# Optimization experiments

Hardware: AMD Instinct MI355X
Metric: run time of the kernel (lower is better)

The kernel has to match this reference:

```python
import jax, jax.numpy as jnp
import numpy as np

N, E, G = 50000, 1600000, 64          # nodes, edges, graphs
NODE_IN, EDGE_IN, HID, L, H = 32, 16, 64, 3, 4
C = HID // H                           # per-head channels (PyG out_channels)


def setup_inputs() -> dict:
    key = jax.random.key(0)
    ks = jax.random.split(key, 12)
    x = jax.random.normal(ks[0], (N, NODE_IN), jnp.float32)
    edge_index = jax.random.randint(ks[1], (2, E), 0, N, jnp.int32)
    edge_attr = jax.random.normal(ks[2], (E, EDGE_IN), jnp.float32)
    batch = jnp.sort(jax.random.randint(ks[3], (N,), 0, G, jnp.int32))
    s = lambda k, shape, fan: jax.random.normal(k, shape, jnp.float32) / np.sqrt(fan)
    Wn = s(ks[4], (NODE_IN, HID), NODE_IN); bn = jnp.zeros((HID,), jnp.float32)
    Wq = s(ks[5], (L, HID, HID), HID);      bq = jnp.zeros((L, HID), jnp.float32)
    Wk = s(ks[6], (L, HID, HID), HID);      bk = jnp.zeros((L, HID), jnp.float32)
    Wv = s(ks[7], (L, HID, HID), HID);      bv = jnp.zeros((L, HID), jnp.float32)
    We = s(ks[8], (L, EDGE_IN, HID), EDGE_IN)          # lin_edge, bias=False in PyG
    Ws = s(ks[9], (L, HID, HID), HID);      bs = jnp.zeros((L, HID), jnp.float32)  # lin_skip
    W1 = s(ks[10], (HID, HID // 2), HID);   b1 = jnp.zeros((HID // 2,), jnp.float32)
    W2 = s(ks[11], (HID // 2, 1), HID // 2); b2 = jnp.zeros((1,), jnp.float32)
    return dict(x=x, edge_index=edge_index, edge_attr=edge_attr, batch=batch,
                Wn=Wn, bn=bn, Wq=Wq, bq=bq, Wk=Wk, bk=bk, Wv=Wv, bv=bv,
                We=We, Ws=Ws, bs=bs, W1=W1, b1=b1, W2=W2, b2=b2)


def _transformer_conv(x, src, dst, edge_attr, Wq, bq, Wk, bk, Wv, bv, We, Ws, bs):
    # PyG TransformerConv (concat=True, beta=False, root_weight=True), eval mode.
    q = (x @ Wq + bq)[dst].reshape(E, H, C)              # query at target nodes
    e = (edge_attr @ We).reshape(E, H, C)                # edge embedding
    k = (x @ Wk + bk)[src].reshape(E, H, C) + e          # key at source + edge
    alpha = (q * k).sum(-1) / jnp.sqrt(jnp.float32(C))   # [E, H]
    amax = jax.ops.segment_max(alpha, dst, num_segments=N)
    ex = jnp.exp(alpha - amax[dst])
    denom = jax.ops.segment_sum(ex, dst, num_segments=N)
    attn = ex / (denom[dst] + 1e-16)                     # segment softmax over in-edges
    v = (x @ Wv + bv)[src].reshape(E, H, C) + e
    agg = jax.ops.segment_sum((v * attn[..., None]).reshape(E, HID), dst, num_segments=N)
    return agg + x @ Ws + bs                             # skip connection (lin_skip)


def reference(x, edge_index, edge_attr, batch, Wn, bn, Wq, bq, Wk, bk, Wv, bv,
              We, Ws, bs, W1, b1, W2, b2):
    src, dst = edge_index[0], edge_index[1]
    h = jax.nn.relu(x @ Wn + bn)
    for l in range(L):  # dropout is identity in eval mode
        h_new = jax.nn.relu(_transformer_conv(h, src, dst, edge_attr,
                                              Wq[l], bq[l], Wk[l], bk[l],
                                              Wv[l], bv[l], We[l], Ws[l], bs[l]))
        h = h + h_new
    # global_mean_pool
    cnt = jax.ops.segment_sum(jnp.ones((N,), h.dtype), batch, num_segments=G)
    pooled = jax.ops.segment_sum(h, batch, num_segments=G) / jnp.maximum(cnt, 1.0)[:, None]
    out = jax.nn.relu(pooled @ W1 + b1) @ W2 + b2
    return out.squeeze(-1)
```

## Files before the change

### kernel.cpp

```cpp
#include <hip/hip_runtime.h>
#include <hip/hip_fp16.h>
#include <stdint.h>

#define Nn 50000
#define Ee 1600000
#define Gg 64
#define TB 2048
#define NTB ((Ee + TB - 1) / TB)
#define NBK ((Nn + 255) / 256)

typedef _Float16 f16x2 __attribute__((ext_vector_type(2)));
typedef _Float16 f16x4 __attribute__((ext_vector_type(4)));

__device__ __forceinline__ float fdot2f(f16x2 a, f16x2 b, float c) {
#if __has_builtin(__builtin_amdgcn_fdot2)
    return __builtin_amdgcn_fdot2(a, b, c, false);
#else
    return fmaf((float)a[0], (float)b[0], fmaf((float)a[1], (float)b[1], c));
#endif
}

__global__ void k_hist(const int* __restrict__ ei, int* __restrict__ deg) {
    int e = blockIdx.x * blockDim.x + threadIdx.x;
    if (e < Ee) atomicAdd(&deg[ei[Ee + e]], 1);
}

__global__ void k_scan1(const int* __restrict__ deg, int* __restrict__ row_ptr,
                        int* __restrict__ bsum) {
    __shared__ int buf[256];
    int i = blockIdx.x * 256 + threadIdx.x;
    int v = (i < Nn) ? deg[i] : 0;
    buf[threadIdx.x] = v;
    __syncthreads();
    for (int off = 1; off < 256; off <<= 1) {
        int t = (threadIdx.x >= off) ? buf[threadIdx.x - off] : 0;
        __syncthreads();
        buf[threadIdx.x] += t;
        __syncthreads();
    }
    if (i < Nn) row_ptr[i + 1] = buf[threadIdx.x];
    if (threadIdx.x == 255) bsum[blockIdx.x] = buf[255];
}

__global__ void k_scan2(int* __restrict__ bsum, int nb) {
    __shared__ int buf[256];
    int v = (threadIdx.x < nb) ? bsum[threadIdx.x] : 0;
    buf[threadIdx.x] = v;
    __syncthreads();
    for (int off = 1; off < 256; off <<= 1) {
        int t = (threadIdx.x >= off) ? buf[threadIdx.x - off] : 0;
        __syncthreads();
        buf[threadIdx.x] += t;
        __syncthreads();
    }
    if (threadIdx.x < nb) bsum[threadIdx.x] = buf[threadIdx.x];
}

__global__ void k_scan3(int* __restrict__ row_ptr, const int* __restrict__ bsum) {
    int i = blockIdx.x * 256 + threadIdx.x;
    if (i > Nn) return;
    if (i == 0) { row_ptr[0] = 0; return; }
    int b = (i - 1) >> 8;
    if (b > 0) row_ptr[i] += bsum[b - 1];
}

__global__ void k_scatter(const int* __restrict__ ei, int* __restrict__ cursor,
                          int* __restrict__ src_perm, int* __restrict__ eperm) {
    int e = blockIdx.x * blockDim.x + threadIdx.x;
    if (e >= Ee) return;
    int dst = ei[Ee + e];
    int pos = atomicAdd(&cursor[dst], 1);
    src_perm[pos] = ei[e];
    eperm[pos] = e;
}

__global__ void k_easort(const float* __restrict__ ea, const int* __restrict__ eperm,
                         __half* __restrict__ ea_h) {
    long t = (long)blockIdx.x * blockDim.x + threadIdx.x;
    if (t >= (long)Ee * 4) return;
    long idx = t >> 2;
    int e = eperm[idx];
    float4 v = ((const float4*)ea)[(long)e * 4 + (t & 3)];
    __half2 lo = __floats2half2_rn(v.x, v.y);
    __half2 hi = __floats2half2_rn(v.z, v.w);
    ((__half2*)ea_h)[t * 2]     = lo;
    ((__half2*)ea_h)[t * 2 + 1] = hi;
}


__global__ __launch_bounds__(256) void k_cnt(const int* __restrict__ ei,
                                             int* __restrict__ table) {
    __shared__ int hist[NBK];
    for (int i = threadIdx.x; i < NBK; i += 256) hist[i] = 0;
    __syncthreads();
    int e0 = blockIdx.x * TB;
    for (int i = threadIdx.x; i < TB; i += 256) {
        int e = e0 + i;
        if (e >= Ee) break;
        atomicAdd(&hist[ei[Ee + e] >> 8], 1);
    }
    __syncthreads();
    for (int i = threadIdx.x; i < NBK; i += 256)
        table[i * NTB + blockIdx.x] = hist[i];
}

__global__ __launch_bounds__(256) void k_colscan(int* __restrict__ table,
                                                 int* __restrict__ bktsz) {
    __shared__ int buf[1024];
    int c = blockIdx.x;
    for (int k = 0; k < 4; ++k) {
        int i = threadIdx.x + k * 256;
        buf[i] = (i < NTB) ? table[c * NTB + i] : 0;
    }
    __syncthreads();
    for (int off = 1; off < 1024; off <<= 1) {
        int v[4];
        for (int k = 0; k < 4; ++k) {
            int i = threadIdx.x + k * 256;
            v[k] = (i >= off) ? buf[i - off] : 0;
        }
        __syncthreads();
        for (int k = 0; k < 4; ++k) buf[threadIdx.x + k * 256] += v[k];
        __syncthreads();
    }
    for (int k = 0; k < 4; ++k) {
        int i = threadIdx.x + k * 256;
        if (i < NTB) table[c * NTB + i] = i ? buf[i - 1] : 0;
    }
    if (threadIdx.x == 0) bktsz[c] = buf[1023];
}

__global__ __launch_bounds__(256) void k_bktscan(const int* __restrict__ bktsz,
                                                 int* __restrict__ bktbase) {
    __shared__ int buf[256];
    int i = threadIdx.x;
    buf[i] = (i < NBK) ? bktsz[i] : 0;
    __syncthreads();
    for (int off = 1; off < 256; off <<= 1) {
        int v = (i >= off) ? buf[i - off] : 0;
        __syncthreads();
        buf[i] += v;
        __syncthreads();
    }
    if (i == 0) bktbase[0] = 0;
    if (i < NBK) bktbase[i + 1] = buf[i];
}

__global__ __launch_bounds__(256) void k_binfill(const int* __restrict__ ei,
                        const int* __restrict__ table, const int* __restrict__ bktbase,
                        unsigned long long* __restrict__ tmp) {
    __shared__ int off_s[NBK];
    __shared__ int cnt_s[NBK];
    for (int i = threadIdx.x; i < NBK; i += 256) {
        off_s[i] = table[i * NTB + blockIdx.x];
        cnt_s[i] = 0;
    }
    __syncthreads();
    int e0 = blockIdx.x * TB;
    for (int i = threadIdx.x; i < TB; i += 256) {
        int e = e0 + i;
        if (e >= Ee) break;
        int src = ei[e];
        int dst = ei[Ee + e];
        int b = dst >> 8;
        int r = atomicAdd(&cnt_s[b], 1);
        long pos = (long)bktbase[b] + off_s[b] + r;
        tmp[pos] = ((unsigned long long)(unsigned)dst << 37)
                 | ((unsigned long long)(unsigned)src << 21)
                 | (unsigned long long)(unsigned)e;
    }
}

__global__ __launch_bounds__(256) void k_bktB(const unsigned long long* __restrict__ tmp,
                        const int* __restrict__ bktbase, int* __restrict__ row_ptr,
                        unsigned long long* __restrict__ tmp2) {
    __shared__ int cnt[256];
    __shared__ int sc[256];
    __shared__ int lro[256];
    int b = blockIdx.x, tid = threadIdx.x;
    cnt[tid] = 0;
    __syncthreads();
    int s = bktbase[b], t_end = bktbase[b + 1];
    for (int i = s + tid; i < t_end; i += 256)
        atomicAdd(&cnt[(int)(tmp[i] >> 37) & 255], 1);
    __syncthreads();
    sc[tid] = cnt[tid];
    __syncthreads();
    for (int off = 1; off < 256; off <<= 1) {
        int v = (tid >= off) ? sc[tid - off] : 0;
        __syncthreads();
        sc[tid] += v;
        __syncthreads();
    }
    lro[tid] = tid ? sc[tid - 1] : 0;
    cnt[tid] = 0;
    int n = b * 256 + tid;
    if (n < Nn) row_ptr[n] = s + lro[tid];
    if (b == NBK - 1 && tid == 0) row_ptr[Nn] = Ee;
    __syncthreads();
    for (int i = s + tid; i < t_end; i += 256) {
        unsigned long long p = tmp[i];
        int dn = (int)(p >> 37) & 255;
        int r = atomicAdd(&cnt[dn], 1);
        int pos = s + lro[dn] + r;
        tmp2[pos] = (((p >> 21) & 0xFFFFull) << 32) | (p & 0x1FFFFFull);
    }
}

__global__ void k_scatB(const unsigned long long* __restrict__ tmp2,
                        int* __restrict__ src_perm,
                        const float* __restrict__ ea, __half* __restrict__ ea_h) {
    int t = blockIdx.x * blockDim.x + threadIdx.x;
    if (t >= Ee) return;
    unsigned long long p = tmp2[t];
    src_perm[t] = (int)(p >> 32);
    int e = (int)(p & 0xFFFFFFFFull);
    const float4* er = (const float4*)(ea + (size_t)e * 16);
    float4 v0 = er[0], v1 = er[1], v2 = er[2], v3 = er[3];
    __half2 h0 = __floats2half2_rn(v0.x, v0.y), h1 = __floats2half2_rn(v0.z, v0.w);
    __half2 h2 = __floats2half2_rn(v1.x, v1.y), h3 = __floats2half2_rn(v1.z, v1.w);
    __half2 h4 = __floats2half2_rn(v2.x, v2.y), h5 = __floats2half2_rn(v2.z, v2.w);
    __half2 h6 = __floats2half2_rn(v3.x, v3.y), h7 = __floats2half2_rn(v3.z, v3.w);
    uint4 a = make_uint4(*(unsigned*)&h0, *(unsigned*)&h1,
                         *(unsigned*)&h2, *(unsigned*)&h3);
    uint4 bb = make_uint4(*(unsigned*)&h4, *(unsigned*)&h5,
                          *(unsigned*)&h6, *(unsigned*)&h7);
    uint4* o = (uint4*)(ea_h + (size_t)t * 16);
    o[0] = a;
    o[1] = bb;
}

__global__ void k_gbound(const int* __restrict__ batch, int* __restrict__ gstart) {
    int n = blockIdx.x * blockDim.x + threadIdx.x;
    if (n >= Nn) return;
    int b = batch[n];
    if (n == 0) { for (int g = 0; g <= b; ++g) gstart[g] = 0; }
    else { int bp = batch[n - 1]; for (int g = bp + 1; g <= b; ++g) gstart[g] = n; }
    if (n == Nn - 1) { for (int g = b + 1; g <= Gg; ++g) gstart[g] = Nn; }
}

__global__ __launch_bounds__(256) void k_encode(const float* __restrict__ x,
                         const float* __restrict__ Wn,
                         const float* __restrict__ bn, float* __restrict__ h) {
    __shared__ float sx[64 * 32];
    int base = blockIdx.x * 64;
    for (int i = threadIdx.x; i < 512; i += 256) {
        int off = i * 4, row = off >> 5;
        float4 v = (base + row < Nn) ? ((const float4*)(x))[(base * 32 + off) >> 2]
                                     : make_float4(0.f, 0.f, 0.f, 0.f);
        ((float4*)sx)[i] = v;
    }
    __syncthreads();
    int lane = threadIdx.x & 63, wv = threadIdx.x >> 6;
    float acc[16];
    float b = bn[lane];
#pragma unroll
    for (int nn = 0; nn < 16; ++nn) acc[nn] = b;
#pragma unroll 1
    for (int k0 = 0; k0 < 32; k0 += 4) {
        float w0 = Wn[(k0 + 0) * 64 + lane];
        float w1 = Wn[(k0 + 1) * 64 + lane];
        float w2 = Wn[(k0 + 2) * 64 + lane];
        float w3 = Wn[(k0 + 3) * 64 + lane];
#pragma unroll
        for (int nn = 0; nn < 16; ++nn) {
            int row = wv * 16 + nn;
            float4 hv = *(const float4*)&sx[row * 32 + k0];
            acc[nn] = fmaf(hv.x, w0, fmaf(hv.y, w1, fmaf(hv.z, w2, fmaf(hv.w, w3, acc[nn]))));
        }
    }
#pragma unroll
    for (int nn = 0; nn < 16; ++nn) {
        int n = base + wv * 16 + nn;
        if (n < Nn) h[(size_t)n * 64 + lane] = fmaxf(acc[nn], 0.f);
    }
}

__global__ void k_wqm3(const float* __restrict__ Wq_all, const float* __restrict__ bq_all,
                       const float* __restrict__ We_all, float* __restrict__ Wqm3,
                       float* __restrict__ bqm3) {
    int l = blockIdx.x;
    const float* Wq = Wq_all + l * 4096;
    const float* bq = bq_all + l * 64;
    const float* We = We_all + l * 1024;
    float* Wqm = Wqm3 + l * 4096;
    float* bqm = bqm3 + l * 64;
    for (int o = threadIdx.x; o < 64 * 64; o += 256) {
        int j = o >> 6, lp = o & 63, hh = lp >> 4, ii = lp & 15;
        float acc = 0.f;
#pragma unroll
        for (int c = 0; c < 16; ++c)
            acc += Wq[j * 64 + hh * 16 + c] * We[ii * 64 + hh * 16 + c];
        Wqm[o] = acc;
    }
    if (threadIdx.x < 64) {
        int hh = threadIdx.x >> 4, ii = threadIdx.x & 15;
        float acc = 0.f;
#pragma unroll
        for (int c = 0; c < 16; ++c)
            acc += bq[hh * 16 + c] * We[ii * 64 + hh * 16 + c];
        bqm[threadIdx.x] = acc;
    }
}

__global__ __launch_bounds__(256) void k_qkvt(const float* __restrict__ h,
                       const float* __restrict__ Wq, const float* __restrict__ bq,
                       const float* __restrict__ Wk, const float* __restrict__ bk,
                       const float* __restrict__ Wv, const float* __restrict__ bv,
                       const float* __restrict__ Wqm, const float* __restrict__ bqm,
                       const float* __restrict__ Ws, const float* __restrict__ bs,
                       float* __restrict__ qn, __half* __restrict__ kv,
                       float* __restrict__ tq, float* __restrict__ sn) {
    __shared__ float sh[64 * 64];
    int base = blockIdx.x * 64;
    for (int i = threadIdx.x; i < 1024; i += 256) {
        int off = i * 4, row = off >> 6;
        float4 v = (base + row < Nn) ? ((const float4*)(h))[((size_t)base * 64 + off) >> 2]
                                     : make_float4(0.f, 0.f, 0.f, 0.f);
        ((float4*)sh)[i] = v;
    }
    __syncthreads();
    int lane = threadIdx.x & 63, wv = threadIdx.x >> 6;
    float aq[16], ak[16], av[16], at[16], as_[16];
    float _bq = bq[lane], _bk = bk[lane], _bv = bv[lane], _bt = bqm[lane], _bs = bs[lane];
#pragma unroll
    for (int nn = 0; nn < 16; ++nn) {
        aq[nn] = _bq; ak[nn] = _bk; av[nn] = _bv; at[nn] = _bt; as_[nn] = _bs;
    }
#pragma unroll 1
    for (int k0 = 0; k0 < 64; k0 += 4) {
        float wq[4], wk[4], wvv[4], wt[4], ws[4];
#pragma unroll
        for (int j = 0; j < 4; ++j) {
            wq[j] = Wq[(k0 + j) * 64 + lane];
            wk[j] = Wk[(k0 + j) * 64 + lane];
            wvv[j] = Wv[(k0 + j) * 64 + lane];
            wt[j] = Wqm[(k0 + j) * 64 + lane];
            ws[j] = Ws[(k0 + j) * 64 + lane];
        }
#pragma unroll
        for (int nn = 0; nn < 16; ++nn) {
            int row = wv * 16 + nn;
            float4 hv = *(const float4*)&sh[row * 64 + k0];
            aq[nn] = fmaf(hv.x, wq[0], fmaf(hv.y, wq[1], fmaf(hv.z, wq[2], fmaf(hv.w, wq[3], aq[nn]))));
            ak[nn] = fmaf(hv.x, wk[0], fmaf(hv.y, wk[1], fmaf(hv.z, wk[2], fmaf(hv.w, wk[3], ak[nn]))));
            av[nn] = fmaf(hv.x, wvv[0], fmaf(hv.y, wvv[1], fmaf(hv.z, wvv[2], fmaf(hv.w, wvv[3], av[nn]))));
            at[nn] = fmaf(hv.x, wt[0], fmaf(hv.y, wt[1], fmaf(hv.z, wt[2], fmaf(hv.w, wt[3], at[nn]))));
            as_[nn] = fmaf(hv.x, ws[0], fmaf(hv.y, ws[1], fmaf(hv.z, ws[2], fmaf(hv.w, ws[3], as_[nn]))));
        }
    }
#pragma unroll
    for (int nn = 0; nn < 16; ++nn) {
        int n = base + wv * 16 + nn;
        if (n < Nn) {
            size_t o = (size_t)n * 64 + lane;
            qn[o] = aq[nn]; tq[o] = at[nn]; sn[o] = as_[nn];
            kv[(size_t)n * 128 + lane]      = __float2half_rn(ak[nn]);
            kv[(size_t)n * 128 + 64 + lane] = __float2half_rn(av[nn]);
        }
    }
}

__global__ __launch_bounds__(256) void k_layer4(float* __restrict__ h,
                      const float* __restrict__ qn, const __half* __restrict__ kv,
                      const float* __restrict__ tq, const float* __restrict__ sn,
                      const int* __restrict__ row_ptr, const int* __restrict__ src_perm,
                      const __half* __restrict__ eah, const float* __restrict__ We) {
    __shared__ float sWe[1024];
    __shared__ float tE[4][64];
    __shared__ float tV[4][64];
    for (int t = threadIdx.x; t < 1024; t += 256) sWe[t] = We[t];
    __syncthreads();
    int lane = threadIdx.x & 63, wv = threadIdx.x >> 6;
    int slot = lane >> 4, sl = lane & 15;
    int n = blockIdx.x * 4 + wv;
    if (n >= Nn) return;
    int beg = row_ptr[n], end = row_ptr[n + 1];
    const float SC = 0.25f * 1.4426950408889634f;
    float4 q4 = *(const float4*)&qn[(size_t)n * 64 + 4 * sl];
    float4 t4 = *(const float4*)&tq[(size_t)n * 64 + 4 * sl];
    f16x2 qa = {(_Float16)(q4.x * SC), (_Float16)(q4.y * SC)};
    f16x2 qb = {(_Float16)(q4.z * SC), (_Float16)(q4.w * SC)};
    f16x2 ta = {(_Float16)(t4.x * SC), (_Float16)(t4.y * SC)};
    f16x2 tb = {(_Float16)(t4.z * SC), (_Float16)(t4.w * SC)};
    const int xoff = 4 * (sl & 3);
    float accd = 0.f;
    float4 accv = make_float4(0.f, 0.f, 0.f, 0.f);
    float4 acce = make_float4(0.f, 0.f, 0.f, 0.f);
    for (int idx = beg; idx < end; idx += 8) {
        int e0 = idx + slot, e1 = idx + 4 + slot;
        bool ok0 = e0 < end, ok1 = e1 < end;
        int i0 = ok0 ? e0 : beg, i1 = ok1 ? e1 : beg;
        int s0 = src_perm[i0], s1 = src_perm[i1];
        f16x4 k0 = *(const f16x4*)(kv + (size_t)s0 * 128 + 4 * sl);
        f16x4 v0 = *(const f16x4*)(kv + (size_t)s0 * 128 + 64 + 4 * sl);
        f16x4 k1 = *(const f16x4*)(kv + (size_t)s1 * 128 + 4 * sl);
        f16x4 v1 = *(const f16x4*)(kv + (size_t)s1 * 128 + 64 + 4 * sl);
        f16x4 x0 = *(const f16x4*)(eah + (size_t)i0 * 16 + xoff);
        f16x4 x1 = *(const f16x4*)(eah + (size_t)i1 * 16 + xoff);
        float a0 = fdot2f(qa, __builtin_shufflevector(k0, k0, 0, 1),
                   fdot2f(qb, __builtin_shufflevector(k0, k0, 2, 3),
                   fdot2f(ta, __builtin_shufflevector(x0, x0, 0, 1),
                   fdot2f(tb, __builtin_shufflevector(x0, x0, 2, 3), -6.0f))));
        float a1 = fdot2f(qa, __builtin_shufflevector(k1, k1, 0, 1),
                   fdot2f(qb, __builtin_shufflevector(k1, k1, 2, 3),
                   fdot2f(ta, __builtin_shufflevector(x1, x1, 0, 1),
                   fdot2f(tb, __builtin_shufflevector(x1, x1, 2, 3), -6.0f))));
        a0 += __shfl_xor(a0, 1, 4); a1 += __shfl_xor(a1, 1, 4);
        a0 += __shfl_xor(a0, 2, 4); a1 += __shfl_xor(a1, 2, 4);
        float p0 = ok0 ? __builtin_exp2f(a0) : 0.f;
        float p1 = ok1 ? __builtin_exp2f(a1) : 0.f;
        accd += p0 + p1;
        accv.x = fmaf(p0, (float)v0[0], fmaf(p1, (float)v1[0], accv.x));
        accv.y = fmaf(p0, (float)v0[1], fmaf(p1, (float)v1[1], accv.y));
        accv.z = fmaf(p0, (float)v0[2], fmaf(p1, (float)v1[2], accv.z));
        accv.w = fmaf(p0, (float)v0[3], fmaf(p1, (float)v1[3], accv.w));
        acce.x = fmaf(p0, (float)x0[0], fmaf(p1, (float)x1[0], acce.x));
        acce.y = fmaf(p0, (float)x0[1], fmaf(p1, (float)x1[1], acce.y));
        acce.z = fmaf(p0, (float)x0[2], fmaf(p1, (float)x1[2], acce.z));
        acce.w = fmaf(p0, (float)x0[3], fmaf(p1, (float)x1[3], acce.w));
    }
    accd   += __shfl_xor(accd, 16);   accd   += __shfl_xor(accd, 32);
    accv.x += __shfl_xor(accv.x, 16); accv.x += __shfl_xor(accv.x, 32);
    accv.y += __shfl_xor(accv.y, 16); accv.y += __shfl_xor(accv.y, 32);
    accv.z += __shfl_xor(accv.z, 16); accv.z += __shfl_xor(accv.z, 32);
    accv.w += __shfl_xor(accv.w, 16); accv.w += __shfl_xor(accv.w, 32);
    acce.x += __shfl_xor(acce.x, 16); acce.x += __shfl_xor(acce.x, 32);
    acce.y += __shfl_xor(acce.y, 16); acce.y += __shfl_xor(acce.y, 32);
    acce.z += __shfl_xor(acce.z, 16); acce.z += __shfl_xor(acce.z, 32);
    acce.w += __shfl_xor(acce.w, 16); acce.w += __shfl_xor(acce.w, 32);
    float inv = 1.f / (accd + 1e-16f);
    if (slot == 0) {
        ((float4*)tE[wv])[sl] = make_float4(acce.x * inv, acce.y * inv,
                                            acce.z * inv, acce.w * inv);
        ((float4*)tV[wv])[sl] = make_float4(accv.x * inv, accv.y * inv,
                                            accv.z * inv, accv.w * inv);
    }
    int hh = lane >> 4;
    float re = 0.f;
#pragma unroll
    for (int i = 0; i < 16; ++i)
        re = fmaf(tE[wv][hh * 16 + i], sWe[i * 64 + lane], re);
    size_t o = (size_t)n * 64 + lane;
    float hv = h[o];
    h[o] = hv + fmaxf(tV[wv][lane] + re + sn[o], 0.f);
}

template <bool SORTED>
__global__ __launch_bounds__(256) void k_layer(float* __restrict__ h,
                      const float* __restrict__ qn, const __half* __restrict__ kv,
                      const float* __restrict__ tq, const float* __restrict__ sn,
                      const int* __restrict__ row_ptr, const int* __restrict__ src_perm,
                      const int* __restrict__ eperm, const __half* __restrict__ eah,
                      const float* __restrict__ eaf, const float* __restrict__ We) {
    __shared__ float sWe[1024];
    __shared__ float tile[4][64];
    for (int t = threadIdx.x; t < 1024; t += 256) sWe[t] = We[t];
    __syncthreads();
    int lane = threadIdx.x & 63, wv = threadIdx.x >> 6;
    int hh = lane >> 4, cc = lane & 15;
    int n = blockIdx.x * 4 + wv;
    if (n >= Nn) return;
    int beg = row_ptr[n], end = row_ptr[n + 1];
    const float SC = 0.25f * 1.4426950408889634f;
    float q = qn[(size_t)n * 64 + lane] * SC;
    float t = tq[(size_t)n * 64 + lane] * SC;
    float m = -INFINITY, accd = 0.f, accv = 0.f, acce = 0.f;
    int idx = beg;
    for (; idx < end; ++idx) {
        long b0 = (long)src_perm[idx] * 128;
        float k0 = __half2float(kv[b0 + lane]);
        float v0 = __half2float(kv[b0 + 64 + lane]);
        float x0 = SORTED ? __half2float(eah[(long)idx * 16 + cc])
                          : eaf[(long)eperm[idx] * 16 + cc];
        float a0 = fmaf(q, k0, x0 * t);
        a0 += __shfl_xor(a0, 1, 16);
        a0 += __shfl_xor(a0, 2, 16);
        a0 += __shfl_xor(a0, 4, 16);
        a0 += __shfl_xor(a0, 8, 16);
        float nm = fmaxf(m, a0);
        float w = __builtin_exp2f(m - nm);
        float p0 = __builtin_exp2f(a0 - nm);
        accd = fmaf(accd, w, p0);
        accv = fmaf(accv, w, p0 * v0);
        acce = fmaf(acce, w, p0 * x0);
        m = nm;
    }
    float inv = 1.f / (accd + 1e-16f);
    tile[wv][lane] = acce * inv;
    float re = 0.f;
#pragma unroll
    for (int i = 0; i < 16; ++i)
        re = fmaf(tile[wv][hh * 16 + i], sWe[i * 64 + lane], re);
    size_t o = (size_t)n * 64 + lane;
    float hv = h[o];
    h[o] = hv + fmaxf(fmaf(accv, inv, re + sn[o]), 0.f);
}

__global__ void k_pool(const float* __restrict__ h, const int* __restrict__ gstart,
                       const float* __restrict__ W1, const float* __restrict__ b1,
                       const float* __restrict__ W2, const float* __restrict__ b2,
                       float* __restrict__ out) {
    int g = blockIdx.x;
    int lane = threadIdx.x & 63, wv = threadIdx.x >> 6;
    int beg = gstart[g], end = gstart[g + 1];
    __shared__ float red[4][64];
    __shared__ float sp[64];
    __shared__ float sh[32];
    float acc = 0.f;
    for (int n = beg + wv; n < end; n += 4) acc += h[(size_t)n * 64 + lane];
    red[wv][lane] = acc;
    __syncthreads();
    if (threadIdx.x < 64) {
        float c = fmaxf((float)(end - beg), 1.f);
        sp[lane] = (red[0][lane] + red[1][lane] + red[2][lane] + red[3][lane]) / c;
    }
    __syncthreads();
    if (threadIdx.x < 32) {
        int t = threadIdx.x;
        float a = b1[t];
#pragma unroll
        for (int i = 0; i < 64; ++i) a = fmaf(sp[i], W1[i * 32 + t], a);
        sh[t] = fmaxf(a, 0.f) * W2[t];
    }
    __syncthreads();
    if (threadIdx.x == 0) {
        float s = b2[0];
#pragma unroll
        for (int i = 0; i < 32; ++i) s += sh[i];
        out[g] = s;
    }
}

extern "C" void kernel_launch(void* const* d_in, const int* in_sizes, int n_in,
                              void* d_out, int out_size, void* d_ws, size_t ws_size,
                              hipStream_t stream) {
    const float* x   = (const float*)d_in[0];
    const int*   ei  = (const int*)d_in[1];
    const float* ea  = (const float*)d_in[2];
    const int*   bat = (const int*)d_in[3];
    const float* Wn  = (const float*)d_in[4];
    const float* bn  = (const float*)d_in[5];
    const float* Wq  = (const float*)d_in[6];
    const float* bq  = (const float*)d_in[7];
    const float* Wk  = (const float*)d_in[8];
    const float* bk  = (const float*)d_in[9];
    const float* Wv  = (const float*)d_in[10];
    const float* bv  = (const float*)d_in[11];
    const float* We  = (const float*)d_in[12];
    const float* Wsk = (const float*)d_in[13];
    const float* bs  = (const float*)d_in[14];
    const float* W1  = (const float*)d_in[15];
    const float* b1  = (const float*)d_in[16];
    const float* W2  = (const float*)d_in[17];
    const float* b2  = (const float*)d_in[18];
    float* out = (float*)d_out;

    const size_t NH = (size_t)Nn * 64;
    float* h    = (float*)d_ws;
    float* qn   = h + NH;
    float* tq   = h + 2 * NH;
    float* sn   = h + 3 * NH;
    __half* kv  = (__half*)(h + 4 * NH);
    float* Wqm3 = h + 5 * NH;
    float* bqm3 = Wqm3 + 3 * 4096;
    int* deg       = (int*)(bqm3 + 3 * 64);
    int* row_ptr   = deg + Nn;
    int* cursor    = row_ptr + Nn + 1;
    int* src_perm  = cursor + Nn;
    int* eperm     = src_perm + Ee;
    int* bsum      = eperm + Ee;
    int* gstart    = bsum + 256;
    char* pe = (char*)(gstart + Gg + 1);
    __half* ea_h = (__half*)(((uintptr_t)pe + 63) & ~(uintptr_t)63);
    char* pt = (char*)(ea_h + (size_t)Ee * 16);
    unsigned long long* tmp =
        (unsigned long long*)(((uintptr_t)pt + 15) & ~(uintptr_t)15);
    size_t need_eah = ((char*)(ea_h + (size_t)Ee * 16)) - (char*)d_ws;
    size_t need_tmp = ((char*)(tmp + Ee)) - (char*)d_ws;
    unsigned long long* tmp2 = (unsigned long long*)qn;
    int* table   = (int*)tq;
    int* bktsz   = (int*)sn;
    int* bktbase = bktsz + 256;
    int mode = (ws_size >= need_tmp) ? 2 : (ws_size >= need_eah) ? 1 : 0;

    if (mode == 2) {
        k_cnt<<<NTB, 256, 0, stream>>>(ei, table);
        k_colscan<<<NBK, 256, 0, stream>>>(table, bktsz);
        k_bktscan<<<1, 256, 0, stream>>>(bktsz, bktbase);
        k_binfill<<<NTB, 256, 0, stream>>>(ei, table, bktbase, tmp);
        k_bktB<<<NBK, 256, 0, stream>>>(tmp, bktbase, row_ptr, tmp2);
        k_scatB<<<(Ee + 255) / 256, 256, 0, stream>>>(tmp2, src_perm, ea, ea_h);
    } else {
        const int NB = 196;
        hipMemsetAsync(deg, 0, Nn * sizeof(int), stream);
        k_hist<<<(Ee + 255) / 256, 256, 0, stream>>>(ei, deg);
        k_scan1<<<NB, 256, 0, stream>>>(deg, row_ptr, bsum);
        k_scan2<<<1, 256, 0, stream>>>(bsum, NB);
        k_scan3<<<(Nn + 256) / 256, 256, 0, stream>>>(row_ptr, bsum);
        hipMemcpyAsync(cursor, row_ptr, Nn * sizeof(int), hipMemcpyDeviceToDevice, stream);
        k_scatter<<<(Ee + 255) / 256, 256, 0, stream>>>(ei, cursor, src_perm, eperm);
        if (mode == 1)
            k_easort<<<((long)Ee * 4 + 255) / 256, 256, 0, stream>>>(ea, eperm, ea_h);
    }
    k_gbound<<<(Nn + 255) / 256, 256, 0, stream>>>(bat, gstart);
    k_wqm3<<<3, 256, 0, stream>>>(Wq, bq, We, Wqm3, bqm3);

    int nodeBlocks = (Nn + 63) / 64;
    k_encode<<<nodeBlocks, 256, 0, stream>>>(x, Wn, bn, h);
    for (int l = 0; l < 3; ++l) {
        k_qkvt<<<nodeBlocks, 256, 0, stream>>>(h, Wq + l * 4096, bq + l * 64,
                                               Wk + l * 4096, bk + l * 64,
                                               Wv + l * 4096, bv + l * 64,
                                               Wqm3 + l * 4096, bqm3 + l * 64,
                                               Wsk + l * 4096, bs + l * 64,
                                               qn, kv, tq, sn);
        if (mode >= 1)
            k_layer4<<<(Nn + 3) / 4, 256, 0, stream>>>(h, qn, kv, tq, sn,
                    row_ptr, src_perm, ea_h, We + l * 1024);
        else
            k_layer<false><<<(Nn + 3) / 4, 256, 0, stream>>>(h, qn, kv, tq, sn,
                    row_ptr, src_perm, eperm, ea_h, ea, We + l * 1024);
    }
    k_pool<<<Gg, 256, 0, stream>>>(h, gstart, W1, b1, W2, b2, out);
}
```

Baseline: 681.4 us.

## Use fp16 packed weights with dot2 in projection and process 4 nodes per wave

Adds a one-time pack kernel that converts the five per-layer projection weights to fp16 in k-pair interleaved layout, with the softmax scale folded into the query weights. The projection kernel then stores h in shared memory as fp16 and accumulates with fdot2. It writes q and the edge-query term as fp16, which halves that traffic and removes per-edge-kernel conversion. The attention kernel now loops over four nodes per wave, so it needs fewer blocks and amortizes the per-block shared-memory load of We. The cost is lower precision in the projections.

Result: faster. 655.6 us (-3.8%).

```diff
diff --git a/kernel.cpp b/kernel.cpp
--- a/kernel.cpp
+++ b/kernel.cpp
@@ -303,50 +303,75 @@
     }
 }
 
-__global__ __launch_bounds__(256) void k_qkvt(const float* __restrict__ h,
-                       const float* __restrict__ Wq, const float* __restrict__ bq,
-                       const float* __restrict__ Wk, const float* __restrict__ bk,
-                       const float* __restrict__ Wv, const float* __restrict__ bv,
-                       const float* __restrict__ Wqm, const float* __restrict__ bqm,
-                       const float* __restrict__ Ws, const float* __restrict__ bs,
-                       float* __restrict__ qn, __half* __restrict__ kv,
-                       float* __restrict__ tq, float* __restrict__ sn) {
-    __shared__ float sh[64 * 64];
+__global__ void k_pack(const float* __restrict__ Wq, const float* __restrict__ Wk,
+                       const float* __restrict__ Wv, const float* __restrict__ Wqm3,
+                       const float* __restrict__ Ws, __half* __restrict__ pw) {
+    int l = blockIdx.x / 5, m = blockIdx.x % 5;
+    const float SC = 0.25f * 1.4426950408889634f;
+    const float* src;
+    float sc = 1.f;
+    if (m == 0)      { src = Wq + l * 4096;   sc = SC; }
+    else if (m == 1) { src = Wk + l * 4096; }
+    else if (m == 2) { src = Wv + l * 4096; }
+    else if (m == 3) { src = Wqm3 + l * 4096; sc = SC; }
+    else             { src = Ws + l * 4096; }
+    __half* dst = pw + ((size_t)l * 5 + m) * 4096;
+    for (int i = threadIdx.x; i < 4096; i += 256) {
+        int k = i >> 6, c = i & 63;
+        dst[(k >> 1) * 128 + 2 * c + (k & 1)] = __float2half_rn(src[i] * sc);
+    }
+}
+
+__global__ __launch_bounds__(256) void k_qkvt2(const float* __restrict__ h,
+                       const __half* __restrict__ pw,
+                       const float* __restrict__ bq, const float* __restrict__ bk,
+                       const float* __restrict__ bv, const float* __restrict__ bqm,
+                       const float* __restrict__ bs,
+                       __half* __restrict__ qn16, __half* __restrict__ kv,
+                       __half* __restrict__ tq16, float* __restrict__ sn) {
+    __shared__ __half sh[64 * 64];
     int base = blockIdx.x * 64;
     for (int i = threadIdx.x; i < 1024; i += 256) {
         int off = i * 4, row = off >> 6;
         float4 v = (base + row < Nn) ? ((const float4*)(h))[((size_t)base * 64 + off) >> 2]
                                      : make_float4(0.f, 0.f, 0.f, 0.f);
-        ((float4*)sh)[i] = v;
+        ((__half2*)sh)[i * 2]     = __floats2half2_rn(v.x, v.y);
+        ((__half2*)sh)[i * 2 + 1] = __floats2half2_rn(v.z, v.w);
     }
     __syncthreads();
     int lane = threadIdx.x & 63, wv = threadIdx.x >> 6;
+    const float SC = 0.25f * 1.4426950408889634f;
+    const __half* Pq = pw;
+    const __half* Pk = pw + 4096;
+    const __half* Pv = pw + 8192;
+    const __half* Pt = pw + 12288;
+    const __half* Ps = pw + 16384;
     float aq[16], ak[16], av[16], at[16], as_[16];
-    float _bq = bq[lane], _bk = bk[lane], _bv = bv[lane], _bt = bqm[lane], _bs = bs[lane];
+    float _bq = bq[lane] * SC, _bk = bk[lane], _bv = bv[lane],
+          _bt = bqm[lane] * SC, _bs = bs[lane];
 #pragma unroll
     for (int nn = 0; nn < 16; ++nn) {
         aq[nn] = _bq; ak[nn] = _bk; av[nn] = _bv; at[nn] = _bt; as_[nn] = _bs;
     }
 #pragma unroll 1
     for (int k0 = 0; k0 < 64; k0 += 4) {
-        float wq[4], wk[4], wvv[4], wt[4], ws[4];
-#pragma unroll
-        for (int j = 0; j < 4; ++j) {
-            wq[j] = Wq[(k0 + j) * 64 + lane];
-            wk[j] = Wk[(k0 + j) * 64 + lane];
-            wvv[j] = Wv[(k0 + j) * 64 + lane];
-            wt[j] = Wqm[(k0 + j) * 64 + lane];
-            ws[j] = Ws[(k0 + j) * 64 + lane];
-        }
+        int pi = (k0 >> 1) * 128 + 2 * lane;
+        f16x2 wq0 = *(const f16x2*)(Pq + pi), wq1 = *(const f16x2*)(Pq + pi + 128);
+        f16x2 wk0 = *(const f16x2*)(Pk + pi), wk1 = *(const f16x2*)(Pk + pi + 128);
+        f16x2 wv0 = *(const f16x2*)(Pv + pi), wv1 = *(const f16x2*)(Pv + pi + 128);
+        f16x2 wt0 = *(const f16x2*)(Pt + pi), wt1 = *(const f16x2*)(Pt + pi + 128);
+        f16x2 ws0 = *(const f16x2*)(Ps + pi), ws1 = *(const f16x2*)(Ps + pi + 128);
 #pragma unroll
         for (int nn = 0; nn < 16; ++nn) {
             int row = wv * 16 + nn;
-            float4 hv = *(const float4*)&sh[row * 64 + k0];
-            aq[nn] = fmaf(hv.x, wq[0], fmaf(hv.y, wq[1], fmaf(hv.z, wq[2], fmaf(hv.w, wq[3], aq[nn]))));
-            ak[nn] = fmaf(hv.x, wk[0], fmaf(hv.y, wk[1], fmaf(hv.z, wk[2], fmaf(hv.w, wk[3], ak[nn]))));
-            av[nn] = fmaf(hv.x, wvv[0], fmaf(hv.y, wvv[1], fmaf(hv.z, wvv[2], fmaf(hv.w, wvv[3], av[nn]))));
-            at[nn] = fmaf(hv.x, wt[0], fmaf(hv.y, wt[1], fmaf(hv.z, wt[2], fmaf(hv.w, wt[3], at[nn]))));
-            as_[nn] = fmaf(hv.x, ws[0], fmaf(hv.y, ws[1], fmaf(hv.z, ws[2], fmaf(hv.w, ws[3], as_[nn]))));
+            f16x4 hv = *(const f16x4*)&sh[row * 64 + k0];
+            f16x2 h01 = __builtin_shufflevector(hv, hv, 0, 1);
+            f16x2 h23 = __builtin_shufflevector(hv, hv, 2, 3);
+            aq[nn]  = fdot2f(h01, wq0, fdot2f(h23, wq1, aq[nn]));
+            ak[nn]  = fdot2f(h01, wk0, fdot2f(h23, wk1, ak[nn]));
+            av[nn]  = fdot2f(h01, wv0, fdot2f(h23, wv1, av[nn]));
+            at[nn]  = fdot2f(h01, wt0, fdot2f(h23, wt1, at[nn]));
+            as_[nn] = fdot2f(h01, ws0, fdot2f(h23, ws1, as_[nn]));
         }
     }
 #pragma unroll
@@ -354,16 +379,18 @@
         int n = base + wv * 16 + nn;
         if (n < Nn) {
             size_t o = (size_t)n * 64 + lane;
-            qn[o] = aq[nn]; tq[o] = at[nn]; sn[o] = as_[nn];
+            qn16[o] = __float2half_rn(aq[nn]);
+            tq16[o] = __float2half_rn(at[nn]);
+            sn[o] = as_[nn];
             kv[(size_t)n * 128 + lane]      = __float2half_rn(ak[nn]);
             kv[(size_t)n * 128 + 64 + lane] = __float2half_rn(av[nn]);
         }
     }
 }
 
-__global__ __launch_bounds__(256) void k_layer4(float* __restrict__ h,
-                      const float* __restrict__ qn, const __half* __restrict__ kv,
-                      const float* __restrict__ tq, const float* __restrict__ sn,
+__global__ __launch_bounds__(256) void k_layer5(float* __restrict__ h,
+                      const __half* __restrict__ qn16, const __half* __restrict__ kv,
+                      const __half* __restrict__ tq16, const float* __restrict__ sn,
                       const int* __restrict__ row_ptr, const int* __restrict__ src_perm,
                       const __half* __restrict__ eah, const float* __restrict__ We) {
     __shared__ float sWe[1024];
@@ -373,86 +400,87 @@
     __syncthreads();
     int lane = threadIdx.x & 63, wv = threadIdx.x >> 6;
     int slot = lane >> 4, sl = lane & 15;
-    int n = blockIdx.x * 4 + wv;
-    if (n >= Nn) return;
-    int beg = row_ptr[n], end = row_ptr[n + 1];
-    const float SC = 0.25f * 1.4426950408889634f;
-    float4 q4 = *(const float4*)&qn[(size_t)n * 64 + 4 * sl];
-    float4 t4 = *(const float4*)&tq[(size_t)n * 64 + 4 * sl];
-    f16x2 qa = {(_Float16)(q4.x * SC), (_Float16)(q4.y * SC)};
-    f16x2 qb = {(_Float16)(q4.z * SC), (_Float16)(q4.w * SC)};
-    f16x2 ta = {(_Float16)(t4.x * SC), (_Float16)(t4.y * SC)};
-    f16x2 tb = {(_Float16)(t4.z * SC), (_Float16)(t4.w * SC)};
+    int hh = lane >> 4;
     const int xoff = 4 * (sl & 3);
-    float accd = 0.f;
-    float4 accv = make_float4(0.f, 0.f, 0.f, 0.f);
-    float4 acce = make_float4(0.f, 0.f, 0.f, 0.f);
-    for (int idx = beg; idx < end; idx += 8) {
-        int e0 = idx + slot, e1 = idx + 4 + slot;
-        bool ok0 = e0 < end, ok1 = e1 < end;
-        int i0 = ok0 ? e0 : beg, i1 = ok1 ? e1 : beg;
-        int s0 = src_perm[i0], s1 = src_perm[i1];
-        f16x4 k0 = *(const f16x4*)(kv + (size_t)s0 * 128 + 4 * sl);
-        f16x4 v0 = *(const f16x4*)(kv + (size_t)s0 * 128 + 64 + 4 * sl);
-        f16x4 k1 = *(const f16x4*)(kv + (size_t)s1 * 128 + 4 * sl);
-        f16x4 v1 = *(const f16x4*)(kv + (size_t)s1 * 128 + 64 + 4 * sl);
-        f16x4 x0 = *(const f16x4*)(eah + (size_t)i0 * 16 + xoff);
-        f16x4 x1 = *(const f16x4*)(eah + (size_t)i1 * 16 + xoff);
-        float a0 = fdot2f(qa, __builtin_shufflevector(k0, k0, 0, 1),
-                   fdot2f(qb, __builtin_shufflevector(k0, k0, 2, 3),
-                   fdot2f(ta, __builtin_shufflevector(x0, x0, 0, 1),
-                   fdot2f(tb, __builtin_shufflevector(x0, x0, 2, 3), -6.0f))));
-        float a1 = fdot2f(qa, __builtin_shufflevector(k1, k1, 0, 1),
-                   fdot2f(qb, __builtin_shufflevector(k1, k1, 2, 3),
-                   fdot2f(ta, __builtin_shufflevector(x1, x1, 0, 1),
-                   fdot2f(tb, __builtin_shufflevector(x1, x1, 2, 3), -6.0f))));
-        a0 += __shfl_xor(a0, 1, 4); a1 += __shfl_xor(a1, 1, 4);
-        a0 += __shfl_xor(a0, 2, 4); a1 += __shfl_xor(a1, 2, 4);
-        float p0 = ok0 ? __builtin_exp2f(a0) : 0.f;
-        float p1 = ok1 ? __builtin_exp2f(a1) : 0.f;
-        accd += p0 + p1;
-        accv.x = fmaf(p0, (float)v0[0], fmaf(p1, (float)v1[0], accv.x));
-        accv.y = fmaf(p0, (float)v0[1], fmaf(p1, (float)v1[1], accv.y));
-        accv.z = fmaf(p0, (float)v0[2], fmaf(p1, (float)v1[2], accv.z));
-        accv.w = fmaf(p0, (float)v0[3], fmaf(p1, (float)v1[3], accv.w));
-        acce.x = fmaf(p0, (float)x0[0], fmaf(p1, (float)x1[0], acce.x));
-        acce.y = fmaf(p0, (float)x0[1], fmaf(p1, (float)x1[1], acce.y));
-        acce.z = fmaf(p0, (float)x0[2], fmaf(p1, (float)x1[2], acce.z));
-        acce.w = fmaf(p0, (float)x0[3], fmaf(p1, (float)x1[3], acce.w));
-    }
-    accd   += __shfl_xor(accd, 16);   accd   += __shfl_xor(accd, 32);
-    accv.x += __shfl_xor(accv.x, 16); accv.x += __shfl_xor(accv.x, 32);
-    accv.y += __shfl_xor(accv.y, 16); accv.y += __shfl_xor(accv.y, 32);
-    accv.z += __shfl_xor(accv.z, 16); accv.z += __shfl_xor(accv.z, 32);
-    accv.w += __shfl_xor(accv.w, 16); accv.w += __shfl_xor(accv.w, 32);
-    acce.x += __shfl_xor(acce.x, 16); acce.x += __shfl_xor(acce.x, 32);
-    acce.y += __shfl_xor(acce.y, 16); acce.y += __shfl_xor(acce.y, 32);
-    acce.z += __shfl_xor(acce.z, 16); acce.z += __shfl_xor(acce.z, 32);
-    acce.w += __shfl_xor(acce.w, 16); acce.w += __shfl_xor(acce.w, 32);
-    float inv = 1.f / (accd + 1e-16f);
-    if (slot == 0) {
-        ((float4*)tE[wv])[sl] = make_float4(acce.x * inv, acce.y * inv,
-                                            acce.z * inv, acce.w * inv);
-        ((float4*)tV[wv])[sl] = make_float4(accv.x * inv, accv.y * inv,
-                                            accv.z * inv, accv.w * inv);
-    }
-    int hh = lane >> 4;
-    float re = 0.f;
-#pragma unroll
-    for (int i = 0; i < 16; ++i)
-        re = fmaf(tE[wv][hh * 16 + i], sWe[i * 64 + lane], re);
-    size_t o = (size_t)n * 64 + lane;
-    float hv = h[o];
-    h[o] = hv + fmaxf(tV[wv][lane] + re + sn[o], 0.f);
-}
-
-template <bool SORTED>
+#pragma unroll 1
+    for (int j = 0; j < 4; ++j) {
+        int n = blockIdx.x * 16 + wv * 4 + j;
+        if (n >= Nn) break;
+        int beg = row_ptr[n], end = row_ptr[n + 1];
+        f16x4 qv = *(const f16x4*)(qn16 + (size_t)n * 64 + 4 * sl);
+        f16x4 tv = *(const f16x4*)(tq16 + (size_t)n * 64 + 4 * sl);
+        f16x2 qa = __builtin_shufflevector(qv, qv, 0, 1);
+        f16x2 qb = __builtin_shufflevector(qv, qv, 2, 3);
+        f16x2 ta = __builtin_shufflevector(tv, tv, 0, 1);
+        f16x2 tb = __builtin_shufflevector(tv, tv, 2, 3);
+        float accd = 0.f;
+        float4 accv = make_float4(0.f, 0.f, 0.f, 0.f);
+        float4 acce = make_float4(0.f, 0.f, 0.f, 0.f);
+        for (int idx = beg; idx < end; idx += 8) {
+            int e0 = idx + slot, e1 = idx + 4 + slot;
+            bool ok0 = e0 < end, ok1 = e1 < end;
+            int i0 = ok0 ? e0 : beg, i1 = ok1 ? e1 : beg;
+            int s0 = src_perm[i0], s1 = src_perm[i1];
+            f16x4 k0 = *(const f16x4*)(kv + (size_t)s0 * 128 + 4 * sl);
+            f16x4 v0 = *(const f16x4*)(kv + (size_t)s0 * 128 + 64 + 4 * sl);
+            f16x4 k1 = *(const f16x4*)(kv + (size_t)s1 * 128 + 4 * sl);
+            f16x4 v1 = *(const f16x4*)(kv + (size_t)s1 * 128 + 64 + 4 * sl);
+            f16x4 x0 = *(const f16x4*)(eah + (size_t)i0 * 16 + xoff);
+            f16x4 x1 = *(const f16x4*)(eah + (size_t)i1 * 16 + xoff);
+            float a0 = fdot2f(qa, __builtin_shufflevector(k0, k0, 0, 1),
+                       fdot2f(qb, __builtin_shufflevector(k0, k0, 2, 3),
+                       fdot2f(ta, __builtin_shufflevector(x0, x0, 0, 1),
+                       fdot2f(tb, __builtin_shufflevector(x0, x0, 2, 3), -6.0f))));
+            float a1 = fdot2f(qa, __builtin_shufflevector(k1, k1, 0, 1),
+                       fdot2f(qb, __builtin_shufflevector(k1, k1, 2, 3),
+                       fdot2f(ta, __builtin_shufflevector(x1, x1, 0, 1),
+                       fdot2f(tb, __builtin_shufflevector(x1, x1, 2, 3), -6.0f))));
+            a0 += __shfl_xor(a0, 1, 4); a1 += __shfl_xor(a1, 1, 4);
+            a0 += __shfl_xor(a0, 2, 4); a1 += __shfl_xor(a1, 2, 4);
+            float p0 = ok0 ? __builtin_exp2f(a0) : 0.f;
+            float p1 = ok1 ? __builtin_exp2f(a1) : 0.f;
+            accd += p0 + p1;
+            accv.x = fmaf(p0, (float)v0[0], fmaf(p1, (float)v1[0], accv.x));
+            accv.y = fmaf(p0, (float)v0[1], fmaf(p1, (float)v1[1], accv.y));
+            accv.z = fmaf(p0, (float)v0[2], fmaf(p1, (float)v1[2], accv.z));
+            accv.w = fmaf(p0, (float)v0[3], fmaf(p1, (float)v1[3], accv.w));
+            acce.x = fmaf(p0, (float)x0[0], fmaf(p1, (float)x1[0], acce.x));
+            acce.y = fmaf(p0, (float)x0[1], fmaf(p1, (float)x1[1], acce.y));
+            acce.z = fmaf(p0, (float)x0[2], fmaf(p1, (float)x1[2], acce.z));
+            acce.w = fmaf(p0, (float)x0[3], fmaf(p1, (float)x1[3], acce.w));
+        }
+        accd   += __shfl_xor(accd, 16);   accd   += __shfl_xor(accd, 32);
+        accv.x += __shfl_xor(accv.x, 16); accv.x += __shfl_xor(accv.x, 32);
+        accv.y += __shfl_xor(accv.y, 16); accv.y += __shfl_xor(accv.y, 32);
+        accv.z += __shfl_xor(accv.z, 16); accv.z += __shfl_xor(accv.z, 32);
+        accv.w += __shfl_xor(accv.w, 16); accv.w += __shfl_xor(accv.w, 32);
+        acce.x += __shfl_xor(acce.x, 16); acce.x += __shfl_xor(acce.x, 32);
+        acce.y += __shfl_xor(acce.y, 16); acce.y += __shfl_xor(acce.y, 32);
+        acce.z += __shfl_xor(acce.z, 16); acce.z += __shfl_xor(acce.z, 32);
+        acce.w += __shfl_xor(acce.w, 16); acce.w += __shfl_xor(acce.w, 32);
+        float inv = 1.f / (accd + 1e-16f);
+        if (slot == 0) {
+            ((float4*)tE[wv])[sl] = make_float4(acce.x * inv, acce.y * inv,
+                                                acce.z * inv, acce.w * inv);
+            ((float4*)tV[wv])[sl] = make_float4(accv.x * inv, accv.y * inv,
+                                                accv.z * inv, accv.w * inv);
+        }
+        float re = 0.f;
+#pragma unroll
+        for (int i = 0; i < 16; ++i)
+            re = fmaf(tE[wv][hh * 16 + i], sWe[i * 64 + lane], re);
+        size_t o = (size_t)n * 64 + lane;
+        float hv = h[o];
+        h[o] = hv + fmaxf(tV[wv][lane] + re + sn[o], 0.f);
+    }
+}
+
 __global__ __launch_bounds__(256) void k_layer(float* __restrict__ h,
-                      const float* __restrict__ qn, const __half* __restrict__ kv,
-                      const float* __restrict__ tq, const float* __restrict__ sn,
+                      const __half* __restrict__ qn16, const __half* __restrict__ kv,
+                      const __half* __restrict__ tq16, const float* __restrict__ sn,
                       const int* __restrict__ row_ptr, const int* __restrict__ src_perm,
-                      const int* __restrict__ eperm, const __half* __restrict__ eah,
-                      const float* __restrict__ eaf, const float* __restrict__ We) {
+                      const int* __restrict__ eperm, const float* __restrict__ eaf,
+                      const float* __restrict__ We) {
     __shared__ float sWe[1024];
     __shared__ float tile[4][64];
     for (int t = threadIdx.x; t < 1024; t += 256) sWe[t] = We[t];
@@ -462,17 +490,15 @@
     int n = blockIdx.x * 4 + wv;
     if (n >= Nn) return;
     int beg = row_ptr[n], end = row_ptr[n + 1];
-    const float SC = 0.25f * 1.4426950408889634f;
-    float q = qn[(size_t)n * 64 + lane] * SC;
-    float t = tq[(size_t)n * 64 + lane] * SC;
+    float q = __half2float(qn16[(size_t)n * 64 + lane]);
+    float t = __half2float(tq16[(size_t)n * 64 + lane]);
     float m = -INFINITY, accd = 0.f, accv = 0.f, acce = 0.f;
     int idx = beg;
     for (; idx < end; ++idx) {
         long b0 = (long)src_perm[idx] * 128;
         float k0 = __half2float(kv[b0 + lane]);
         float v0 = __half2float(kv[b0 + 64 + lane]);
-        float x0 = SORTED ? __half2float(eah[(long)idx * 16 + cc])
-                          : eaf[(long)eperm[idx] * 16 + cc];
+        float x0 = eaf[(long)eperm[idx] * 16 + cc];
         float a0 = fmaf(q, k0, x0 * t);
         a0 += __shfl_xor(a0, 1, 16);
         a0 += __shfl_xor(a0, 2, 16);
@@ -564,7 +590,8 @@
     __half* kv  = (__half*)(h + 4 * NH);
     float* Wqm3 = h + 5 * NH;
     float* bqm3 = Wqm3 + 3 * 4096;
-    int* deg       = (int*)(bqm3 + 3 * 64);
+    __half* pw  = (__half*)(bqm3 + 3 * 64);
+    int* deg       = (int*)(pw + 3 * 5 * 4096);
     int* row_ptr   = deg + Nn;
     int* cursor    = row_ptr + Nn + 1;
     int* src_perm  = cursor + Nn;
@@ -582,6 +609,8 @@
     int* table   = (int*)tq;
     int* bktsz   = (int*)sn;
     int* bktbase = bktsz + 256;
+    __half* qn16 = (__half*)qn;
+    __half* tq16 = (__half*)tq;
     int mode = (ws_size >= need_tmp) ? 2 : (ws_size >= need_eah) ? 1 : 0;
 
     if (mode == 2) {
@@ -605,22 +634,21 @@
     }
     k_gbound<<<(Nn + 255) / 256, 256, 0, stream>>>(bat, gstart);
     k_wqm3<<<3, 256, 0, stream>>>(Wq, bq, We, Wqm3, bqm3);
+    k_pack<<<15, 256, 0, stream>>>(Wq, Wk, Wv, Wqm3, Wsk, pw);
 
     int nodeBlocks = (Nn + 63) / 64;
     k_encode<<<nodeBlocks, 256, 0, stream>>>(x, Wn, bn, h);
     for (int l = 0; l < 3; ++l) {
-        k_qkvt<<<nodeBlocks, 256, 0, stream>>>(h, Wq + l * 4096, bq + l * 64,
-                                               Wk + l * 4096, bk + l * 64,
-                                               Wv + l * 4096, bv + l * 64,
-                                               Wqm3 + l * 4096, bqm3 + l * 64,
-                                               Wsk + l * 4096, bs + l * 64,
-                                               qn, kv, tq, sn);
+        k_qkvt2<<<nodeBlocks, 256, 0, stream>>>(h, pw + (size_t)l * 5 * 4096,
+                                                bq + l * 64, bk + l * 64, bv + l * 64,
+                                                bqm3 + l * 64, bs + l * 64,
+                                                qn16, kv, tq16, sn);
         if (mode >= 1)
-            k_layer4<<<(Nn + 3) / 4, 256, 0, stream>>>(h, qn, kv, tq, sn,
+            k_layer5<<<(Nn + 15) / 16, 256, 0, stream>>>(h, qn16, kv, tq16, sn,
                     row_ptr, src_perm, ea_h, We + l * 1024);
         else
-            k_layer<false><<<(Nn + 3) / 4, 256, 0, stream>>>(h, qn, kv, tq, sn,
-                    row_ptr, src_perm, eperm, ea_h, ea, We + l * 1024);
+            k_layer<<<(Nn + 3) / 4, 256, 0, stream>>>(h, qn16, kv, tq16, sn,
+                    row_ptr, src_perm, eperm, ea, We + l * 1024);
     }
     k_pool<<<Gg, 256, 0, stream>>>(h, gstart, W1, b1, W2, b2, out);
 }
```
